# Kernel tuning notes

Measured on AMD Instinct MI355X. Metric: run time of the kernel, lower is better.

## Reference

```python
import jax, jax.numpy as jnp
import numpy as np

L = 3          # num_layers
HID = 256      # hidden_size
NF = 16        # num_features_params
TF = NF + 1    # total_features
B = 128
T = 256
EPS = 1e-5     # torch LayerNorm default


def _ln(x, g, b):
    mu = jnp.mean(x, axis=-1, keepdims=True)
    var = jnp.mean((x - mu) ** 2, axis=-1, keepdims=True)
    return (x - mu) * jax.lax.rsqrt(var + EPS) * g + b


def setup_inputs() -> dict:
    key = jax.random.key(0)
    ks = iter(jax.random.split(key, 64))
    w = lambda *s: jax.random.normal(next(ks), s, dtype=jnp.float32) * 0.05
    d = {
        'parameters_input': jax.random.normal(next(ks), (B, NF), dtype=jnp.float32),
        'displacement_input': jax.random.normal(next(ks), (B, T), dtype=jnp.float32),
        # input_embed: Linear(TF,H) + LayerNorm(H)
        'embed_w': w(TF, HID), 'embed_b': w(HID),
        'embed_g': jnp.ones((HID,), jnp.float32), 'embed_beta': jnp.zeros((HID,), jnp.float32),
        # skip_connection: Linear(TF, H//2)
        'skip_w': w(TF, HID // 2), 'skip_b': w(HID // 2),
        # per-layer LSTM cell params, stacked over L
        'gates_w': w(L, 2 * HID, 4 * HID), 'gates_b': w(L, 4 * HID),
        'inln_g': jnp.ones((L, HID), jnp.float32), 'inln_b': jnp.zeros((L, HID), jnp.float32),
        'hln_g': jnp.ones((L, HID), jnp.float32), 'hln_b': jnp.zeros((L, HID), jnp.float32),
        'sln_g': jnp.ones((L, HID), jnp.float32), 'sln_b': jnp.zeros((L, HID), jnp.float32),
        'aw1': w(L, HID, HID), 'ab1': w(L, HID),
        'aw2': w(L, HID, 1), 'ab2': w(L, 1),
        # per-layer residual blocks: Linear(H,2H), Linear(2H,H), LayerNorm(H)
        'rw1': w(L, HID, 2 * HID), 'rb1': w(L, 2 * HID),
        'rw2': w(L, 2 * HID, HID), 'rb2': w(L, HID),
        'rln_g': jnp.ones((L, HID), jnp.float32), 'rln_b': jnp.zeros((L, HID), jnp.float32),
        # output head: Linear(H + H//2, H//2) [bug-fixed in_features], LayerNorm, Linear(H//2,1)
        'ow1': w(HID + HID // 2, HID // 2), 'ob1': w(HID // 2),
        'oln_g': jnp.ones((HID // 2,), jnp.float32), 'oln_b': jnp.zeros((HID // 2,), jnp.float32),
        'ow2': w(HID // 2, 1), 'ob2': w(1),
    }
    return d


def _forward(parameters_input, displacement_input, embed_w, embed_b, embed_g, embed_beta,
             skip_w, skip_b, gates_w, gates_b, inln_g, inln_b, hln_g, hln_b, sln_g, sln_b,
             aw1, ab1, aw2, ab2, rw1, rb1, rw2, rb2, rln_g, rln_b,
             ow1, ob1, oln_g, oln_b, ow2, ob2):
    Bb, Tt = displacement_input.shape
    # [B,T,TF]: displacement as extra feature at index 0, params broadcast over time
    seq = jnp.concatenate([
        displacement_input[..., None],
        jnp.broadcast_to(parameters_input[:, None, :], (Bb, Tt, parameters_input.shape[1])),
    ], axis=-1)
    xs = jnp.swapaxes(seq, 0, 1)  # [T,B,TF]
    h0 = jnp.zeros((L, Bb, HID), seq.dtype)
    c0 = jnp.zeros((L, Bb, HID), seq.dtype)

    def step(carry, xt):
        h_all, c_all = carry
        skip = jax.nn.relu(xt @ skip_w + skip_b)                      # [B,H/2]
        x = jax.nn.relu(_ln(xt @ embed_w + embed_b, embed_g, embed_beta))
        hs, cs = [], []
        for l in range(L):
            residual = x
            h, c = h_all[l], c_all[l]
            xn = _ln(x, inln_g[l], inln_b[l])
            hn = _ln(h, hln_g[l], hln_b[l])
            g4 = jnp.concatenate([xn, hn], axis=-1) @ gates_w[l] + gates_b[l]
            i, f, g, o = jnp.split(g4, 4, axis=-1)
            i = jax.nn.sigmoid(i); f = jax.nn.sigmoid(f)
            g = jnp.tanh(g); o = jax.nn.sigmoid(o)
            imp = jax.nn.sigmoid(jnp.tanh(c @ aw1[l] + ab1[l]) @ aw2[l] + ab2[l])  # [B,1]
            c = _ln((f * c + i * g) * imp, sln_g[l], sln_b[l])
            h = o * jnp.tanh(c)
            hs.append(h); cs.append(c)
            x = h
            rb = jax.nn.relu(x @ rw1[l] + rb1[l]) @ rw2[l] + rb2[l]
            x = _ln(rb + x, rln_g[l], rln_b[l]) + residual
        y = jnp.concatenate([x, skip], axis=-1)                        # [B, H + H/2]
        out = jax.nn.relu(_ln(y @ ow1 + ob1, oln_g, oln_b)) @ ow2 + ob2  # [B,1]
        return (jnp.stack(hs), jnp.stack(cs)), out[:, 0]

    _, outs = jax.lax.scan(step, (h0, c0), xs)   # outs [T,B]
    return jnp.swapaxes(outs, 0, 1)              # [B,T]


def reference(parameters_input, displacement_input, embed_w, embed_b, embed_g, embed_beta,
              skip_w, skip_b, gates_w, gates_b, inln_g, inln_b, hln_g, hln_b, sln_g, sln_b,
              aw1, ab1, aw2, ab2, rw1, rb1, rw2, rb2, rln_g, rln_b,
              ow1, ob1, oln_g, oln_b, ow2, ob2):
    return _forward(parameters_input, displacement_input, embed_w, embed_b, embed_g, embed_beta,
                    skip_w, skip_b, gates_w, gates_b, inln_g, inln_b, hln_g, hln_b, sln_g, sln_b,
                    aw1, ab1, aw2, ab2, rw1, rb1, rw2, rb2, rln_g, rln_b,
                    ow1, ob1, oln_g, oln_b, ow2, ob2)
```

## Files before the change

kernel.cpp:

```cpp
#include <hip/hip_runtime.h>
#include <cstdint>

#define TT 256
#define HH 256
#define LL 3
#define NTH 512
#define SWG 8
#define CLN 32
#define RW 4
#define LN_EPS 1e-5f
#define ACTSTRIDE 16384


__device__ __forceinline__ float fast_sigmoid(float x) {
    return 1.f / (1.f + __expf(-x));
}
__device__ __forceinline__ float fast_tanh(float x) {
    float xc = fminf(fmaxf(x, -15.f), 15.f);
    float e = __expf(2.f * xc);
    return 1.f - 2.f / (e + 1.f);
}
__device__ __forceinline__ float relu(float x) { return fmaxf(x, 0.f); }

__device__ __forceinline__ void cst(float* p, float v) {
    __hip_atomic_store(p, v, __ATOMIC_RELAXED, __HIP_MEMORY_SCOPE_AGENT);
}
__device__ __forceinline__ float cld(const float* p) {
    return __hip_atomic_load(p, __ATOMIC_RELAXED, __HIP_MEMORY_SCOPE_AGENT);
}

__device__ __forceinline__ float4 rowsum4(float s0, float q0, float s1, float q1,
                                          float* scr, int tid) {
#pragma unroll
    for (int o = 32; o > 0; o >>= 1) {
        s0 += __shfl_down(s0, o); q0 += __shfl_down(q0, o);
        s1 += __shfl_down(s1, o); q1 += __shfl_down(q1, o);
    }
    int w = tid >> 6;
    if ((tid & 63) == 0) { scr[w*4] = s0; scr[w*4+1] = q0; scr[w*4+2] = s1; scr[w*4+3] = q1; }
    __syncthreads();
    int base = (tid >> 8) * 16;
    float sA = 0, qA = 0, sB = 0, qB = 0;
#pragma unroll
    for (int i = 0; i < 4; i++) {
        sA += scr[base + i*4];     qA += scr[base + i*4 + 1];
        sB += scr[base + i*4 + 2]; qB += scr[base + i*4 + 3];
    }
    __syncthreads();
    return make_float4(sA, qA, sB, qB);
}

__device__ __forceinline__ void fma16(float4 w, float4 x,
                                      float4& a0, float4& a1, float4& a2, float4& a3) {
    a0.x = fmaf(w.x, x.x, a0.x); a0.y = fmaf(w.y, x.x, a0.y);
    a0.z = fmaf(w.z, x.x, a0.z); a0.w = fmaf(w.w, x.x, a0.w);
    a1.x = fmaf(w.x, x.y, a1.x); a1.y = fmaf(w.y, x.y, a1.y);
    a1.z = fmaf(w.z, x.y, a1.z); a1.w = fmaf(w.w, x.y, a1.w);
    a2.x = fmaf(w.x, x.z, a2.x); a2.y = fmaf(w.y, x.z, a2.y);
    a2.z = fmaf(w.z, x.z, a2.z); a2.w = fmaf(w.w, x.z, a2.w);
    a3.x = fmaf(w.x, x.w, a3.x); a3.y = fmaf(w.y, x.w, a3.y);
    a3.z = fmaf(w.z, x.w, a3.z); a3.w = fmaf(w.w, x.w, a3.w);
}


struct Args {
    const float *params, *disp;
    const float *embed_b, *embed_g, *embed_beta;
    const float *skip_b;
    const float *gates_b;
    const float *inln_g, *inln_b, *hln_g, *hln_b, *sln_g, *sln_b;
    const float *ab1, *aw2, *ab2;
    const float *rb1, *rb2, *rln_g, *rln_b;
    const float *ob1, *oln_g, *oln_b, *ow2, *ob2;
    const float *gw, *a1w, *r1w, *r2w, *ew, *sw, *o1w;
    float* out;
    float* act;
    int* bar;
};

__global__ __launch_bounds__(NTH) void xlstm_kernel(Args A) {
    const int tid = threadIdx.x;
    const int cid = blockIdx.x & 31;
    const int m   = blockIdx.x >> 5;
    const int n   = tid & 255;
    const int p   = tid >> 8;
    const int rA = p, rB = p + 2;

    float* gatesB = A.act + (size_t)cid * ACTSTRIDE;
    float* a1B  = gatesB + 4096;
    float* r2P  = gatesB + 4224;
    int* cnt = A.bar + cid * 128;

    __shared__ __align__(16) float4 P4[2064];
    __shared__ __align__(16) float4 xnhnT[512];
    __shared__ __align__(16) float4 cT4[256];
    __shared__ __align__(16) float4 hT4[256];
    __shared__ __align__(16) float4 xT4[256];
    __shared__ __align__(16) float4 skT4[128];
    __shared__ __align__(16) float4 r1locT[64];
    __shared__ float xtT[17 * 4];
    __shared__ float scr[64];

    float x2[2] = {0.f, 0.f};
    float h2[LL][2] = {{0.f,0.f},{0.f,0.f},{0.f,0.f}};
    float c2[LL][2] = {{0.f,0.f},{0.f,0.f},{0.f,0.f}};

    int ep = 0;
    auto csig = [&]() {
        ep++;
        __syncthreads();
        if (tid == 0)
            __hip_atomic_fetch_add(cnt, 1, __ATOMIC_RELAXED, __HIP_MEMORY_SCOPE_AGENT);
    };
    auto cwait = [&]() {
        if (tid == 0) {
            while (__hip_atomic_load(cnt, __ATOMIC_RELAXED, __HIP_MEMORY_SCOPE_AGENT) < SWG * ep)
                __builtin_amdgcn_s_sleep(4);
            asm volatile("" ::: "memory");
        }
        __syncthreads();
    };

    if (tid < 64) {
        int k = tid >> 2, rr = tid & 3;
        xtT[(1 + k) * 4 + rr] = A.params[(RW * cid + rr) * 16 + k];
    }
    if (tid < 4) xtT[tid] = A.disp[(RW * cid + tid) * TT + 0];
    __syncthreads();

    for (int t = 0; t < TT; t++) {
        float e0 = A.embed_b[n], e1 = e0;
#pragma unroll 4
        for (int k = 0; k < 17; k++) {
            float w = A.ew[k * 256 + n];
            e0 = fmaf(w, xtT[k * 4 + rA], e0);
            e1 = fmaf(w, xtT[k * 4 + rB], e1);
        }
        {
            int mm = tid & 127, q = tid >> 7;
            float s = A.skip_b[mm];
#pragma unroll 4
            for (int k = 0; k < 17; k++) s = fmaf(A.sw[k * 128 + mm], xtT[k * 4 + q], s);
            ((float*)&skT4[mm])[q] = relu(s);
        }
        float4 rs = rowsum4(e0, e0 * e0, e1, e1 * e1, scr, tid);
        {
            float mu = rs.x * (1.f/HH), inv = rsqrtf(rs.y * (1.f/HH) - mu*mu + LN_EPS);
            x2[0] = relu((e0 - mu) * inv * A.embed_g[n] + A.embed_beta[n]);
            mu = rs.z * (1.f/HH); inv = rsqrtf(rs.w * (1.f/HH) - mu*mu + LN_EPS);
            x2[1] = relu((e1 - mu) * inv * A.embed_g[n] + A.embed_beta[n]);
        }

#pragma unroll 1
        for (int l = 0; l < LL; l++) {
            rs = rowsum4(x2[0], x2[0]*x2[0], x2[1], x2[1]*x2[1], scr, tid);
            {
                const float* g = A.inln_g + l*HH; const float* b = A.inln_b + l*HH;
                float mu = rs.x*(1.f/HH), inv = rsqrtf(rs.y*(1.f/HH) - mu*mu + LN_EPS);
                ((float*)&xnhnT[n])[rA] = (x2[0] - mu) * inv * g[n] + b[n];
                mu = rs.z*(1.f/HH); inv = rsqrtf(rs.w*(1.f/HH) - mu*mu + LN_EPS);
                ((float*)&xnhnT[n])[rB] = (x2[1] - mu) * inv * g[n] + b[n];
            }
            float hA = h2[l][0], hB = h2[l][1];
            rs = rowsum4(hA, hA*hA, hB, hB*hB, scr, tid);
            {
                const float* g = A.hln_g + l*HH; const float* b = A.hln_b + l*HH;
                float mu = rs.x*(1.f/HH), inv = rsqrtf(rs.y*(1.f/HH) - mu*mu + LN_EPS);
                ((float*)&xnhnT[256 + n])[rA] = (hA - mu) * inv * g[n] + b[n];
                mu = rs.z*(1.f/HH); inv = rsqrtf(rs.w*(1.f/HH) - mu*mu + LN_EPS);
                ((float*)&xnhnT[256 + n])[rB] = (hB - mu) * inv * g[n] + b[n];
            }
            ((float*)&cT4[n])[rA] = c2[l][0];
            ((float*)&cT4[n])[rB] = c2[l][1];
            __syncthreads();

            {
                int j = tid & 31, kg = tid >> 5;
                const float4* Wq = (const float4*)A.gw + (size_t)l*512*256 + (m*32 + j);
                float4 a0={0,0,0,0}, a1v={0,0,0,0}, a2={0,0,0,0}, a3={0,0,0,0};
                int k0 = kg * 32;
#pragma unroll 8
                for (int kk = 0; kk < 32; kk++) {
                    int k = k0 + kk;
                    fma16(Wq[(size_t)k * 256], xnhnT[k], a0, a1v, a2, a3);
                }
                int b = kg*32 + j;
                P4[b] = a0; P4[516 + b] = a1v; P4[2*516 + b] = a2; P4[3*516 + b] = a3;
            }
            __syncthreads();
            if (tid < 128) {
                int j2 = tid >> 2, row = tid & 3;
                float4 s = {0,0,0,0};
#pragma unroll
                for (int kg = 0; kg < 16; kg++) {
                    float4 v = P4[row*516 + kg*32 + j2];
                    s.x += v.x; s.y += v.y; s.z += v.z; s.w += v.w;
                }
                float* d = gatesB + row*1024 + m*128 + j2*4;
                cst(d+0, s.x); cst(d+1, s.y); cst(d+2, s.z); cst(d+3, s.w);
            }
            __syncthreads();
            if (tid < 256) {
                int j = tid & 7, kg = tid >> 3;
                const float4* Wq = (const float4*)A.a1w + (size_t)l*256*64 + (m*8 + j);
                float4 a0={0,0,0,0}, a1v={0,0,0,0}, a2={0,0,0,0}, a3={0,0,0,0};
                int k0 = kg * 8;
#pragma unroll
                for (int kk = 0; kk < 8; kk++) {
                    int k = k0 + kk;
                    fma16(Wq[(size_t)k * 64], cT4[k], a0, a1v, a2, a3);
                }
                int b = kg*8 + j;
                P4[b] = a0; P4[260 + b] = a1v; P4[2*260 + b] = a2; P4[3*260 + b] = a3;
            }
            __syncthreads();
            if (tid < 32) {
                int j2 = tid >> 2, row = tid & 3;
                float4 s = {0,0,0,0};
#pragma unroll
                for (int kg = 0; kg < 32; kg++) {
                    float4 v = P4[row*260 + kg*8 + j2];
                    s.x += v.x; s.y += v.y; s.z += v.z; s.w += v.w;
                }
                const float* ab1p = A.ab1 + l*HH + m*32 + j2*4;
                const float* aw2p = A.aw2 + l*HH + m*32 + j2*4;
                float d = fast_tanh(s.x + ab1p[0]) * aw2p[0]
                        + fast_tanh(s.y + ab1p[1]) * aw2p[1]
                        + fast_tanh(s.z + ab1p[2]) * aw2p[2]
                        + fast_tanh(s.w + ab1p[3]) * aw2p[3];
                scr[tid] = d;
            }
            __syncthreads();
            if (tid < 4) {
                float s = 0.f;
#pragma unroll
                for (int j2 = 0; j2 < 8; j2++) s += scr[j2*4 + tid];
                cst(a1B + m*4 + tid, s);
            }

            float4 w2[8], w3[8];
            csig();
            {
                int j = tid & 15, kg = tid >> 4, k0 = kg * 8;
                const float4* Wq = (const float4*)A.r1w + (size_t)l*256*128 + (m*16 + j);
#pragma unroll
                for (int kk = 0; kk < 8; kk++) w2[kk] = Wq[(size_t)(k0 + kk) * 128];
                int j3 = tid & 63, kg3 = tid >> 6, k03 = kg3 * 8;
                const float4* Wq3 = (const float4*)A.r2w + (size_t)l*512*64
                                    + (size_t)(m*64) * 64 + j3;
#pragma unroll
                for (int kk = 0; kk < 8; kk++) w3[kk] = Wq3[(size_t)(k03 + kk) * 64];
            }
            cwait();

            float imp0, imp1;
            {
                float sA = A.ab2[l], sB = A.ab2[l];
#pragma unroll
                for (int mm = 0; mm < SWG; mm++) {
                    sA += cld(a1B + mm*4 + rA);
                    sB += cld(a1B + mm*4 + rB);
                }
                imp0 = fast_sigmoid(sA); imp1 = fast_sigmoid(sB);
            }
            const float* gb = A.gates_b + l*1024;
            float craw0, craw1, og0, og1;
            {
                const float* go = gatesB + rA*1024;
                float ii = fast_sigmoid(cld(go + n) + gb[n]);
                float ff = fast_sigmoid(cld(go + 256 + n) + gb[256+n]);
                float gg = fast_tanh(cld(go + 512 + n) + gb[512+n]);
                og0 = fast_sigmoid(cld(go + 768 + n) + gb[768+n]);
                craw0 = (ff * c2[l][0] + ii * gg) * imp0;
            }
            {
                const float* go = gatesB + rB*1024;
                float ii = fast_sigmoid(cld(go + n) + gb[n]);
                float ff = fast_sigmoid(cld(go + 256 + n) + gb[256+n]);
                float gg = fast_tanh(cld(go + 512 + n) + gb[512+n]);
                og1 = fast_sigmoid(cld(go + 768 + n) + gb[768+n]);
                craw1 = (ff * c2[l][1] + ii * gg) * imp1;
            }
            rs = rowsum4(craw0, craw0*craw0, craw1, craw1*craw1, scr, tid);
            {
                const float* g = A.sln_g + l*HH; const float* b = A.sln_b + l*HH;
                float mu = rs.x*(1.f/HH), inv = rsqrtf(rs.y*(1.f/HH) - mu*mu + LN_EPS);
                float cn = (craw0 - mu) * inv * g[n] + b[n];
                c2[l][0] = cn; float hh = og0 * fast_tanh(cn);
                h2[l][0] = hh; ((float*)&hT4[n])[rA] = hh;
                mu = rs.z*(1.f/HH); inv = rsqrtf(rs.w*(1.f/HH) - mu*mu + LN_EPS);
                cn = (craw1 - mu) * inv * g[n] + b[n];
                c2[l][1] = cn; hh = og1 * fast_tanh(cn);
                h2[l][1] = hh; ((float*)&hT4[n])[rB] = hh;
            }
            __syncthreads();

            {
                int j = tid & 15, kg = tid >> 4;
                float4 a0={0,0,0,0}, a1v={0,0,0,0}, a2={0,0,0,0}, a3={0,0,0,0};
                int k0 = kg * 8;
#pragma unroll
                for (int kk = 0; kk < 8; kk++)
                    fma16(w2[kk], hT4[k0 + kk], a0, a1v, a2, a3);
                int b = kg*16 + j;
                P4[b] = a0; P4[516 + b] = a1v; P4[2*516 + b] = a2; P4[3*516 + b] = a3;
            }
            __syncthreads();
            if (tid < 64) {
                int j2 = tid >> 2, row = tid & 3;
                float4 s = {0,0,0,0};
#pragma unroll
                for (int kg = 0; kg < 32; kg++) {
                    float4 v = P4[row*516 + kg*16 + j2];
                    s.x += v.x; s.y += v.y; s.z += v.z; s.w += v.w;
                }
                const float* rb1p = A.rb1 + l*512 + m*64 + j2*4;
                ((float*)&r1locT[j2*4 + 0])[row] = relu(s.x + rb1p[0]);
                ((float*)&r1locT[j2*4 + 1])[row] = relu(s.y + rb1p[1]);
                ((float*)&r1locT[j2*4 + 2])[row] = relu(s.z + rb1p[2]);
                ((float*)&r1locT[j2*4 + 3])[row] = relu(s.w + rb1p[3]);
            }
            __syncthreads();

            {
                int j = tid & 63, kg = tid >> 6;
                float4 a0={0,0,0,0}, a1v={0,0,0,0}, a2={0,0,0,0}, a3={0,0,0,0};
                int k0 = kg * 8;
#pragma unroll
                for (int kk = 0; kk < 8; kk++) {
                    int lk = k0 + kk;
                    fma16(w3[kk], r1locT[lk], a0, a1v, a2, a3);
                }
                int b = kg*64 + j;
                P4[b] = a0; P4[516 + b] = a1v; P4[2*516 + b] = a2; P4[3*516 + b] = a3;
            }
            __syncthreads();
            {
                int j2 = tid >> 2, row = tid & 3;
                if (tid < 256) {
                    float4 s = {0,0,0,0};
#pragma unroll
                    for (int kg = 0; kg < 8; kg++) {
                        float4 v = P4[row*516 + kg*64 + j2];
                        s.x += v.x; s.y += v.y; s.z += v.z; s.w += v.w;
                    }
                    float* d = r2P + m*1024 + row*256 + j2*4;
                    cst(d+0, s.x); cst(d+1, s.y); cst(d+2, s.z); cst(d+3, s.w);
                }
            }
            csig(); cwait();

            const float* rb2p = A.rb2 + l*HH;
            float s0 = rb2p[n] + h2[l][0];
            float s1 = rb2p[n] + h2[l][1];
#pragma unroll
            for (int mm = 0; mm < SWG; mm++) {
                s0 += cld(r2P + mm*1024 + rA*256 + n);
                s1 += cld(r2P + mm*1024 + rB*256 + n);
            }
            rs = rowsum4(s0, s0*s0, s1, s1*s1, scr, tid);
            {
                const float* g = A.rln_g + l*HH; const float* b = A.rln_b + l*HH;
                float mu = rs.x*(1.f/HH), inv = rsqrtf(rs.y*(1.f/HH) - mu*mu + LN_EPS);
                x2[0] = (s0 - mu) * inv * g[n] + b[n] + x2[0];
                mu = rs.z*(1.f/HH); inv = rsqrtf(rs.w*(1.f/HH) - mu*mu + LN_EPS);
                x2[1] = (s1 - mu) * inv * g[n] + b[n] + x2[1];
            }
        }

        ((float*)&xT4[n])[rA] = x2[0];
        ((float*)&xT4[n])[rB] = x2[1];
        if (tid < 4 && t < TT - 1)
            xtT[tid] = A.disp[(RW * cid + tid) * TT + t + 1];
        __syncthreads();
        {
            int j = tid & 31, z = tid >> 5;
            int row = z & 3, kg = z >> 2;
            const float4* W4 = (const float4*)A.o1w;
            float4 a4 = {0,0,0,0};
            int k0 = kg * 96;
#pragma unroll 8
            for (int kk = 0; kk < 96; kk++) {
                int k = k0 + kk;
                float xv = (k < 256) ? ((const float*)&xT4[k])[row]
                                     : ((const float*)&skT4[k - 256])[row];
                float4 w = W4[(size_t)k * 32 + j];
                a4.x = fmaf(w.x, xv, a4.x); a4.y = fmaf(w.y, xv, a4.y);
                a4.z = fmaf(w.z, xv, a4.z); a4.w = fmaf(w.w, xv, a4.w);
            }
            P4[z * 33 + j] = a4;
        }
        __syncthreads();
        if (tid < 128) {
            int j = tid & 31, row = tid >> 5;
            float4 v = {0,0,0,0};
#pragma unroll
            for (int kg = 0; kg < 4; kg++) {
                float4 pv = P4[(kg * 4 + row) * 33 + j];
                v.x += pv.x; v.y += pv.y; v.z += pv.z; v.w += pv.w;
            }
            float4 b1 = ((const float4*)A.ob1)[j];
            v.x += b1.x; v.y += b1.y; v.z += b1.z; v.w += b1.w;
            float s = v.x + v.y + v.z + v.w;
            float q = v.x*v.x + v.y*v.y + v.z*v.z + v.w*v.w;
#pragma unroll
            for (int o = 16; o > 0; o >>= 1) { s += __shfl_down(s, o); q += __shfl_down(q, o); }
            s = __shfl(s, tid & 32);
            q = __shfl(q, tid & 32);
            float mu = s * (1.f/128.f);
            float inv = rsqrtf(q * (1.f/128.f) - mu*mu + LN_EPS);
            float4 g4 = ((const float4*)A.oln_g)[j];
            float4 be4 = ((const float4*)A.oln_b)[j];
            float4 w24 = ((const float4*)A.ow2)[j];
            float part = relu((v.x - mu) * inv * g4.x + be4.x) * w24.x
                       + relu((v.y - mu) * inv * g4.y + be4.y) * w24.y
                       + relu((v.z - mu) * inv * g4.z + be4.z) * w24.z
                       + relu((v.w - mu) * inv * g4.w + be4.w) * w24.w;
#pragma unroll
            for (int o = 16; o > 0; o >>= 1) part += __shfl_down(part, o);
            if (m == 0 && (tid & 31) == 0)
                A.out[(RW*cid + row) * TT + t] = part + A.ob2[0];
        }
        __syncthreads();
    }
}


extern "C" void kernel_launch(void* const* d_in, const int* in_sizes, int n_in,
                              void* d_out, int out_size, void* d_ws, size_t ws_size,
                              hipStream_t stream) {
    hipMemsetAsync(d_ws, 0, CLN * 128 * sizeof(int), stream);

    Args A;
    A.params     = (const float*)d_in[0];
    A.disp       = (const float*)d_in[1];
    A.ew         = (const float*)d_in[2];
    A.embed_b    = (const float*)d_in[3];
    A.embed_g    = (const float*)d_in[4];
    A.embed_beta = (const float*)d_in[5];
    A.sw         = (const float*)d_in[6];
    A.skip_b     = (const float*)d_in[7];
    A.gw         = (const float*)d_in[8];
    A.gates_b    = (const float*)d_in[9];
    A.inln_g     = (const float*)d_in[10];
    A.inln_b     = (const float*)d_in[11];
    A.hln_g      = (const float*)d_in[12];
    A.hln_b      = (const float*)d_in[13];
    A.sln_g      = (const float*)d_in[14];
    A.sln_b      = (const float*)d_in[15];
    A.a1w        = (const float*)d_in[16];
    A.ab1        = (const float*)d_in[17];
    A.aw2        = (const float*)d_in[18];
    A.ab2        = (const float*)d_in[19];
    A.r1w        = (const float*)d_in[20];
    A.rb1        = (const float*)d_in[21];
    A.r2w        = (const float*)d_in[22];
    A.rb2        = (const float*)d_in[23];
    A.rln_g      = (const float*)d_in[24];
    A.rln_b      = (const float*)d_in[25];
    A.o1w        = (const float*)d_in[26];
    A.ob1        = (const float*)d_in[27];
    A.oln_g      = (const float*)d_in[28];
    A.oln_b      = (const float*)d_in[29];
    A.ow2        = (const float*)d_in[30];
    A.ob2        = (const float*)d_in[31];
    A.out        = (float*)d_out;
    A.bar        = (int*)d_ws;
    A.act        = (float*)d_ws + CLN * 128;

    xlstm_kernel<<<CLN * SWG, NTH, 0, stream>>>(A);
}
```

Baseline: 23.27 ms.

## Double block size to 1024 threads with one batch row per thread

Raises threads per block from 512 to 1024 so each thread handles one batch row instead of two. The K dimension of every GEMV-style partial sum is split more finely, and the partial-sum buffer and reduction loops are resized to match. The aim is to cut per-thread serial work and the latency of each recurrent step. In exchange, the cross-thread reductions grow longer, the kernel uses more shared memory, and register pressure under launch_bounds 1024 may rise.

```diff
diff --git a/kernel.cpp b/kernel.cpp
--- a/kernel.cpp
+++ b/kernel.cpp
@@ -4,12 +4,13 @@
 #define TT 256
 #define HH 256
 #define LL 3
-#define NTH 512
+#define NTH 1024
 #define SWG 8
 #define CLN 32
 #define RW 4
 #define LN_EPS 1e-5f
 #define ACTSTRIDE 16384
+#define PL1 1028
 
 
 __device__ __forceinline__ float fast_sigmoid(float x) {
@@ -29,25 +30,21 @@
     return __hip_atomic_load(p, __ATOMIC_RELAXED, __HIP_MEMORY_SCOPE_AGENT);
 }
 
-__device__ __forceinline__ float4 rowsum4(float s0, float q0, float s1, float q1,
-                                          float* scr, int tid) {
-#pragma unroll
-    for (int o = 32; o > 0; o >>= 1) {
-        s0 += __shfl_down(s0, o); q0 += __shfl_down(q0, o);
-        s1 += __shfl_down(s1, o); q1 += __shfl_down(q1, o);
-    }
+__device__ __forceinline__ float2 rowsum2(float s, float q, float* scr, int tid) {
+#pragma unroll
+    for (int o = 32; o > 0; o >>= 1) { s += __shfl_down(s, o); q += __shfl_down(q, o); }
     int w = tid >> 6;
-    if ((tid & 63) == 0) { scr[w*4] = s0; scr[w*4+1] = q0; scr[w*4+2] = s1; scr[w*4+3] = q1; }
+    if ((tid & 63) == 0) { scr[w*2] = s; scr[w*2+1] = q; }
     __syncthreads();
-    int base = (tid >> 8) * 16;
-    float sA = 0, qA = 0, sB = 0, qB = 0;
+    int r = tid >> 8;
+    float ss = 0.f, qq = 0.f;
 #pragma unroll
     for (int i = 0; i < 4; i++) {
-        sA += scr[base + i*4];     qA += scr[base + i*4 + 1];
-        sB += scr[base + i*4 + 2]; qB += scr[base + i*4 + 3];
+        ss += scr[(r*4 + i)*2];
+        qq += scr[(r*4 + i)*2 + 1];
     }
     __syncthreads();
-    return make_float4(sA, qA, sB, qB);
+    return make_float2(ss, qq);
 }
 
 __device__ __forceinline__ void fma16(float4 w, float4 x,
@@ -83,15 +80,14 @@
     const int cid = blockIdx.x & 31;
     const int m   = blockIdx.x >> 5;
     const int n   = tid & 255;
-    const int p   = tid >> 8;
-    const int rA = p, rB = p + 2;
+    const int r   = tid >> 8;
 
     float* gatesB = A.act + (size_t)cid * ACTSTRIDE;
     float* a1B  = gatesB + 4096;
     float* r2P  = gatesB + 4224;
     int* cnt = A.bar + cid * 128;
 
-    __shared__ __align__(16) float4 P4[2064];
+    __shared__ __align__(16) float4 P4[4 * PL1];
     __shared__ __align__(16) float4 xnhnT[512];
     __shared__ __align__(16) float4 cT4[256];
     __shared__ __align__(16) float4 hT4[256];
@@ -101,9 +97,9 @@
     __shared__ float xtT[17 * 4];
     __shared__ float scr[64];
 
-    float x2[2] = {0.f, 0.f};
-    float h2[LL][2] = {{0.f,0.f},{0.f,0.f},{0.f,0.f}};
-    float c2[LL][2] = {{0.f,0.f},{0.f,0.f},{0.f,0.f}};
+    float x1 = 0.f;
+    float h1[LL] = {0.f, 0.f, 0.f};
+    float c1[LL] = {0.f, 0.f, 0.f};
 
     int ep = 0;
     auto csig = [&]() {
@@ -129,71 +125,61 @@
     __syncthreads();
 
     for (int t = 0; t < TT; t++) {
-        float e0 = A.embed_b[n], e1 = e0;
+        float e0 = A.embed_b[n];
 #pragma unroll 4
-        for (int k = 0; k < 17; k++) {
-            float w = A.ew[k * 256 + n];
-            e0 = fmaf(w, xtT[k * 4 + rA], e0);
-            e1 = fmaf(w, xtT[k * 4 + rB], e1);
-        }
+        for (int k = 0; k < 17; k++)
+            e0 = fmaf(A.ew[k * 256 + n], xtT[k * 4 + r], e0);
         {
-            int mm = tid & 127, q = tid >> 7;
+            int mm = tid & 127, q = (tid >> 7) & 3;
             float s = A.skip_b[mm];
 #pragma unroll 4
             for (int k = 0; k < 17; k++) s = fmaf(A.sw[k * 128 + mm], xtT[k * 4 + q], s);
             ((float*)&skT4[mm])[q] = relu(s);
         }
-        float4 rs = rowsum4(e0, e0 * e0, e1, e1 * e1, scr, tid);
+        float2 rs = rowsum2(e0, e0 * e0, scr, tid);
         {
             float mu = rs.x * (1.f/HH), inv = rsqrtf(rs.y * (1.f/HH) - mu*mu + LN_EPS);
-            x2[0] = relu((e0 - mu) * inv * A.embed_g[n] + A.embed_beta[n]);
-            mu = rs.z * (1.f/HH); inv = rsqrtf(rs.w * (1.f/HH) - mu*mu + LN_EPS);
-            x2[1] = relu((e1 - mu) * inv * A.embed_g[n] + A.embed_beta[n]);
+            x1 = relu((e0 - mu) * inv * A.embed_g[n] + A.embed_beta[n]);
         }
 
 #pragma unroll 1
         for (int l = 0; l < LL; l++) {
-            rs = rowsum4(x2[0], x2[0]*x2[0], x2[1], x2[1]*x2[1], scr, tid);
+            rs = rowsum2(x1, x1 * x1, scr, tid);
             {
                 const float* g = A.inln_g + l*HH; const float* b = A.inln_b + l*HH;
                 float mu = rs.x*(1.f/HH), inv = rsqrtf(rs.y*(1.f/HH) - mu*mu + LN_EPS);
-                ((float*)&xnhnT[n])[rA] = (x2[0] - mu) * inv * g[n] + b[n];
-                mu = rs.z*(1.f/HH); inv = rsqrtf(rs.w*(1.f/HH) - mu*mu + LN_EPS);
-                ((float*)&xnhnT[n])[rB] = (x2[1] - mu) * inv * g[n] + b[n];
-            }
-            float hA = h2[l][0], hB = h2[l][1];
-            rs = rowsum4(hA, hA*hA, hB, hB*hB, scr, tid);
+                ((float*)&xnhnT[n])[r] = (x1 - mu) * inv * g[n] + b[n];
+            }
+            float hA = h1[l];
+            rs = rowsum2(hA, hA * hA, scr, tid);
             {
                 const float* g = A.hln_g + l*HH; const float* b = A.hln_b + l*HH;
                 float mu = rs.x*(1.f/HH), inv = rsqrtf(rs.y*(1.f/HH) - mu*mu + LN_EPS);
-                ((float*)&xnhnT[256 + n])[rA] = (hA - mu) * inv * g[n] + b[n];
-                mu = rs.z*(1.f/HH); inv = rsqrtf(rs.w*(1.f/HH) - mu*mu + LN_EPS);
-                ((float*)&xnhnT[256 + n])[rB] = (hB - mu) * inv * g[n] + b[n];
-            }
-            ((float*)&cT4[n])[rA] = c2[l][0];
-            ((float*)&cT4[n])[rB] = c2[l][1];
+                ((float*)&xnhnT[256 + n])[r] = (hA - mu) * inv * g[n] + b[n];
+            }
+            ((float*)&cT4[n])[r] = c1[l];
             __syncthreads();
 
             {
                 int j = tid & 31, kg = tid >> 5;
                 const float4* Wq = (const float4*)A.gw + (size_t)l*512*256 + (m*32 + j);
                 float4 a0={0,0,0,0}, a1v={0,0,0,0}, a2={0,0,0,0}, a3={0,0,0,0};
-                int k0 = kg * 32;
+                int k0 = kg * 16;
 #pragma unroll 8
-                for (int kk = 0; kk < 32; kk++) {
+                for (int kk = 0; kk < 16; kk++) {
                     int k = k0 + kk;
                     fma16(Wq[(size_t)k * 256], xnhnT[k], a0, a1v, a2, a3);
                 }
                 int b = kg*32 + j;
-                P4[b] = a0; P4[516 + b] = a1v; P4[2*516 + b] = a2; P4[3*516 + b] = a3;
+                P4[b] = a0; P4[PL1 + b] = a1v; P4[2*PL1 + b] = a2; P4[3*PL1 + b] = a3;
             }
             __syncthreads();
             if (tid < 128) {
                 int j2 = tid >> 2, row = tid & 3;
                 float4 s = {0,0,0,0};
 #pragma unroll
-                for (int kg = 0; kg < 16; kg++) {
-                    float4 v = P4[row*516 + kg*32 + j2];
+                for (int kg = 0; kg < 32; kg++) {
+                    float4 v = P4[row*PL1 + kg*32 + j2];
                     s.x += v.x; s.y += v.y; s.z += v.z; s.w += v.w;
                 }
                 float* d = gatesB + row*1024 + m*128 + j2*4;
@@ -238,80 +224,65 @@
                 cst(a1B + m*4 + tid, s);
             }
 
-            float4 w2[8], w3[8];
+            float4 w2[4], w3[4];
             csig();
             {
-                int j = tid & 15, kg = tid >> 4, k0 = kg * 8;
+                int j = tid & 15, kg = tid >> 4, k0 = kg * 4;
                 const float4* Wq = (const float4*)A.r1w + (size_t)l*256*128 + (m*16 + j);
 #pragma unroll
-                for (int kk = 0; kk < 8; kk++) w2[kk] = Wq[(size_t)(k0 + kk) * 128];
-                int j3 = tid & 63, kg3 = tid >> 6, k03 = kg3 * 8;
+                for (int kk = 0; kk < 4; kk++) w2[kk] = Wq[(size_t)(k0 + kk) * 128];
+                int j3 = tid & 63, kg3 = tid >> 6, k03 = kg3 * 4;
                 const float4* Wq3 = (const float4*)A.r2w + (size_t)l*512*64
                                     + (size_t)(m*64) * 64 + j3;
 #pragma unroll
-                for (int kk = 0; kk < 8; kk++) w3[kk] = Wq3[(size_t)(k03 + kk) * 64];
+                for (int kk = 0; kk < 4; kk++) w3[kk] = Wq3[(size_t)(k03 + kk) * 64];
             }
             cwait();
 
-            float imp0, imp1;
-            {
-                float sA = A.ab2[l], sB = A.ab2[l];
-#pragma unroll
-                for (int mm = 0; mm < SWG; mm++) {
-                    sA += cld(a1B + mm*4 + rA);
-                    sB += cld(a1B + mm*4 + rB);
-                }
-                imp0 = fast_sigmoid(sA); imp1 = fast_sigmoid(sB);
+            float imp0;
+            {
+                float sA = A.ab2[l];
+#pragma unroll
+                for (int mm = 0; mm < SWG; mm++) sA += cld(a1B + mm*4 + r);
+                imp0 = fast_sigmoid(sA);
             }
             const float* gb = A.gates_b + l*1024;
-            float craw0, craw1, og0, og1;
-            {
-                const float* go = gatesB + rA*1024;
+            float craw0, og0;
+            {
+                const float* go = gatesB + r*1024;
                 float ii = fast_sigmoid(cld(go + n) + gb[n]);
                 float ff = fast_sigmoid(cld(go + 256 + n) + gb[256+n]);
                 float gg = fast_tanh(cld(go + 512 + n) + gb[512+n]);
                 og0 = fast_sigmoid(cld(go + 768 + n) + gb[768+n]);
-                craw0 = (ff * c2[l][0] + ii * gg) * imp0;
-            }
-            {
-                const float* go = gatesB + rB*1024;
-                float ii = fast_sigmoid(cld(go + n) + gb[n]);
-                float ff = fast_sigmoid(cld(go + 256 + n) + gb[256+n]);
-                float gg = fast_tanh(cld(go + 512 + n) + gb[512+n]);
-                og1 = fast_sigmoid(cld(go + 768 + n) + gb[768+n]);
-                craw1 = (ff * c2[l][1] + ii * gg) * imp1;
-            }
-            rs = rowsum4(craw0, craw0*craw0, craw1, craw1*craw1, scr, tid);
+                craw0 = (ff * c1[l] + ii * gg) * imp0;
+            }
+            rs = rowsum2(craw0, craw0*craw0, scr, tid);
             {
                 const float* g = A.sln_g + l*HH; const float* b = A.sln_b + l*HH;
                 float mu = rs.x*(1.f/HH), inv = rsqrtf(rs.y*(1.f/HH) - mu*mu + LN_EPS);
                 float cn = (craw0 - mu) * inv * g[n] + b[n];
-                c2[l][0] = cn; float hh = og0 * fast_tanh(cn);
-                h2[l][0] = hh; ((float*)&hT4[n])[rA] = hh;
-                mu = rs.z*(1.f/HH); inv = rsqrtf(rs.w*(1.f/HH) - mu*mu + LN_EPS);
-                cn = (craw1 - mu) * inv * g[n] + b[n];
-                c2[l][1] = cn; hh = og1 * fast_tanh(cn);
-                h2[l][1] = hh; ((float*)&hT4[n])[rB] = hh;
+                c1[l] = cn; float hh = og0 * fast_tanh(cn);
+                h1[l] = hh; ((float*)&hT4[n])[r] = hh;
             }
             __syncthreads();
 
             {
                 int j = tid & 15, kg = tid >> 4;
                 float4 a0={0,0,0,0}, a1v={0,0,0,0}, a2={0,0,0,0}, a3={0,0,0,0};
-                int k0 = kg * 8;
-#pragma unroll
-                for (int kk = 0; kk < 8; kk++)
+                int k0 = kg * 4;
+#pragma unroll
+                for (int kk = 0; kk < 4; kk++)
                     fma16(w2[kk], hT4[k0 + kk], a0, a1v, a2, a3);
                 int b = kg*16 + j;
-                P4[b] = a0; P4[516 + b] = a1v; P4[2*516 + b] = a2; P4[3*516 + b] = a3;
+                P4[b] = a0; P4[PL1 + b] = a1v; P4[2*PL1 + b] = a2; P4[3*PL1 + b] = a3;
             }
             __syncthreads();
             if (tid < 64) {
                 int j2 = tid >> 2, row = tid & 3;
                 float4 s = {0,0,0,0};
 #pragma unroll
-                for (int kg = 0; kg < 32; kg++) {
-                    float4 v = P4[row*516 + kg*16 + j2];
+                for (int kg = 0; kg < 64; kg++) {
+                    float4 v = P4[row*PL1 + kg*16 + j2];
                     s.x += v.x; s.y += v.y; s.z += v.z; s.w += v.w;
                 }
                 const float* rb1p = A.rb1 + l*512 + m*64 + j2*4;
@@ -325,14 +296,14 @@
             {
                 int j = tid & 63, kg = tid >> 6;
                 float4 a0={0,0,0,0}, a1v={0,0,0,0}, a2={0,0,0,0}, a3={0,0,0,0};
-                int k0 = kg * 8;
-#pragma unroll
-                for (int kk = 0; kk < 8; kk++) {
+                int k0 = kg * 4;
+#pragma unroll
+                for (int kk = 0; kk < 4; kk++) {
                     int lk = k0 + kk;
                     fma16(w3[kk], r1locT[lk], a0, a1v, a2, a3);
                 }
                 int b = kg*64 + j;
-                P4[b] = a0; P4[516 + b] = a1v; P4[2*516 + b] = a2; P4[3*516 + b] = a3;
+                P4[b] = a0; P4[PL1 + b] = a1v; P4[2*PL1 + b] = a2; P4[3*PL1 + b] = a3;
             }
             __syncthreads();
             {
@@ -340,8 +311,8 @@
                 if (tid < 256) {
                     float4 s = {0,0,0,0};
 #pragma unroll
-                    for (int kg = 0; kg < 8; kg++) {
-                        float4 v = P4[row*516 + kg*64 + j2];
+                    for (int kg = 0; kg < 16; kg++) {
+                        float4 v = P4[row*PL1 + kg*64 + j2];
                         s.x += v.x; s.y += v.y; s.z += v.z; s.w += v.w;
                     }
                     float* d = r2P + m*1024 + row*256 + j2*4;
@@ -351,25 +322,19 @@
             csig(); cwait();
 
             const float* rb2p = A.rb2 + l*HH;
-            float s0 = rb2p[n] + h2[l][0];
-            float s1 = rb2p[n] + h2[l][1];
-#pragma unroll
-            for (int mm = 0; mm < SWG; mm++) {
-                s0 += cld(r2P + mm*1024 + rA*256 + n);
-                s1 += cld(r2P + mm*1024 + rB*256 + n);
-            }
-            rs = rowsum4(s0, s0*s0, s1, s1*s1, scr, tid);
+            float s0 = rb2p[n] + h1[l];
+#pragma unroll
+            for (int mm = 0; mm < SWG; mm++)
+                s0 += cld(r2P + mm*1024 + r*256 + n);
+            rs = rowsum2(s0, s0*s0, scr, tid);
             {
                 const float* g = A.rln_g + l*HH; const float* b = A.rln_b + l*HH;
                 float mu = rs.x*(1.f/HH), inv = rsqrtf(rs.y*(1.f/HH) - mu*mu + LN_EPS);
-                x2[0] = (s0 - mu) * inv * g[n] + b[n] + x2[0];
-                mu = rs.z*(1.f/HH); inv = rsqrtf(rs.w*(1.f/HH) - mu*mu + LN_EPS);
-                x2[1] = (s1 - mu) * inv * g[n] + b[n] + x2[1];
-            }
-        }
-
-        ((float*)&xT4[n])[rA] = x2[0];
-        ((float*)&xT4[n])[rB] = x2[1];
+                x1 = (s0 - mu) * inv * g[n] + b[n] + x1;
+            }
+        }
+
+        ((float*)&xT4[n])[r] = x1;
         if (tid < 4 && t < TT - 1)
             xtT[tid] = A.disp[(RW * cid + tid) * TT + t + 1];
         __syncthreads();
@@ -378,9 +343,9 @@
             int row = z & 3, kg = z >> 2;
             const float4* W4 = (const float4*)A.o1w;
             float4 a4 = {0,0,0,0};
-            int k0 = kg * 96;
+            int k0 = kg * 48;
 #pragma unroll 8
-            for (int kk = 0; kk < 96; kk++) {
+            for (int kk = 0; kk < 48; kk++) {
                 int k = k0 + kk;
                 float xv = (k < 256) ? ((const float*)&xT4[k])[row]
                                      : ((const float*)&skT4[k - 256])[row];
@@ -395,7 +360,7 @@
             int j = tid & 31, row = tid >> 5;
             float4 v = {0,0,0,0};
 #pragma unroll
-            for (int kg = 0; kg < 4; kg++) {
+            for (int kg = 0; kg < 8; kg++) {
                 float4 pv = P4[(kg * 4 + row) * 33 + j];
                 v.x += pv.x; v.y += pv.y; v.z += pv.z; v.w += pv.w;
             }
```

New measurement: 31.87 ms. 37.0% more time.
